# Kernel tuning notes

Measured on AMD Instinct MI355X. Metric: run time of the kernel, lower is better.

The kernel has to match this reference:

```python
import jax, jax.numpy as jnp
import numpy as np

EPS = 1e-5

def _bn(x, gamma, beta):
    # training-mode BatchNorm1d over (batch, points) per channel; x: [B, C, N]
    mean = x.mean(axis=(0, 2), keepdims=True)
    var = x.var(axis=(0, 2), keepdims=True)
    return gamma[None, :, None] * (x - mean) * jax.lax.rsqrt(var + EPS) + beta[None, :, None]

def _conv_nn(x, idx, W, b):
    # x: [B, Cin, N_in]; idx: [N_out, k]; W: [Cout, Cin, k]
    g = x[:, :, idx]  # gather -> [B, Cin, N_out, k]
    return jnp.einsum('bink,oik->bon', g, W) + b[None, :, None]

def setup_inputs() -> dict:
    key = jax.random.key(0)
    ks = jax.random.split(key, 8)
    B, Cin, Cout = 32, 32, 64
    Nin, Nout, K, KP = 32768, 8192, 9, 4
    s = 0.05
    return {
        'x': jax.random.normal(ks[0], (B, Cin, Nin), jnp.float32),
        'W1': jax.random.normal(ks[1], (Cout, Cin, K), jnp.float32) * s,
        'b1': jnp.zeros((Cout,), jnp.float32),
        'W2': jax.random.normal(ks[2], (Cout, Cout, K), jnp.float32) * s,
        'b2': jnp.zeros((Cout,), jnp.float32),
        'We': jax.random.normal(ks[3], (Cout, Cin), jnp.float32) * s,
        'be': jnp.zeros((Cout,), jnp.float32),
        'g1': jnp.ones((Cout,), jnp.float32), 'beta1': jnp.zeros((Cout,), jnp.float32),
        'g2': jnp.ones((Cout,), jnp.float32), 'beta2': jnp.zeros((Cout,), jnp.float32),
        'g3': jnp.ones((Cout,), jnp.float32), 'beta3': jnp.zeros((Cout,), jnp.float32),
        'idx1': jax.random.randint(ks[4], (Nout, K), 0, Nin, jnp.int32),
        'idx2': jax.random.randint(ks[5], (Nout, K), 0, Nout, jnp.int32),
        'pool_idx': jax.random.randint(ks[6], (Nout, KP), 0, Nin, jnp.int32),
    }

def reference(x, W1, b1, W2, b2, We, be, g1, beta1, g2, beta2, g3, beta3, idx1, idx2, pool_idx):
    # main branch: ConvNN -> BN -> ReLU -> ConvNN -> BN
    out = jax.nn.relu(_bn(_conv_nn(x, idx1, W1, b1), g1, beta1))
    out = _bn(_conv_nn(out, idx2, W2, b2), g2, beta2)
    # shortcut: AvgPoolNN (k=4) -> 1x1 conv expand -> BN
    pooled = x[:, :, pool_idx].mean(axis=-1)  # [B, Cin, N_out]
    identity = _bn(jnp.einsum('bin,oi->bon', pooled, We) + be[None, :, None], g3, beta3)
    return jax.nn.relu(out + identity)
```

## Files before the change

kernel.cpp:

```cpp
#include <hip/hip_runtime.h>

typedef __attribute__((ext_vector_type(8))) short short8_t;
typedef __attribute__((ext_vector_type(4))) float f32x4_t;

#define NOUT 8192
#define NIN 32768
#define MTOT 262144.0f
#define ST_STRIPES 64

static __device__ __forceinline__ float bf2f(ushort u) {
    union { float f; unsigned int i; } x; x.i = ((unsigned int)u) << 16; return x.f;
}
static __device__ __forceinline__ ushort f2bf(float f) {
    union { float f; unsigned int i; } x; x.f = f;
    unsigned int r = x.i + 0x7fffu + ((x.i >> 16) & 1u);
    return (ushort)(r >> 16);
}

__global__ __launch_bounds__(256) void transpose_x_kernel(
    const float* __restrict__ x, ushort* __restrict__ xt)
{
    __shared__ ushort T[64][66];
    const int tid = threadIdx.x;
    const int n0 = blockIdx.x * 64, c0 = blockIdx.y * 64;
    const int lane64 = tid & 63, rb = (tid >> 6) * 16;
    #pragma unroll
    for (int r = 0; r < 16; ++r) {
        int c_l = rb + r;
        T[c_l][lane64] = f2bf(x[(size_t)(c0 + c_l) * NIN + n0 + lane64]);
    }
    __syncthreads();
    #pragma unroll
    for (int r = 0; r < 16; ++r) {
        int n_l = rb + r;
        xt[(size_t)(n0 + n_l) * 1024 + c0 + lane64] = T[lane64][n_l];
    }
}

__global__ __launch_bounds__(256) void prep_w_kernel(
    const float* __restrict__ W1, const float* __restrict__ W2,
    const float* __restrict__ We,
    ushort* __restrict__ w1p, ushort* __restrict__ w2p, ushort* __restrict__ wep)
{
    int t = blockIdx.x * 256 + threadIdx.x;
    const int N1 = 9 * 64 * 32, N2 = 9 * 64 * 64, N3 = 64 * 32;
    if (t < N1) {
        int k = t >> 11, rem = t & 2047, o = rem >> 5, i = rem & 31;
        w1p[t] = f2bf(W1[o * 288 + i * 9 + k]);
    } else if (t < N1 + N2) {
        int t2 = t - N1;
        int k = t2 >> 12, rem = t2 & 4095, o = rem >> 6, ci = rem & 63;
        w2p[t2] = f2bf(W2[o * 576 + ci * 9 + k]);
    } else if (t < N1 + N2 + N3) {
        int t3 = t - N1 - N2;
        wep[t3] = f2bf(We[t3]);
    }
}

__global__ __launch_bounds__(256) void conv1_kernel(
    const ushort* __restrict__ xt, const int* __restrict__ idx1,
    const ushort* __restrict__ w1p, ushort* __restrict__ out1,
    float* __restrict__ st)
{
    __shared__ ushort As[128 * 40];
    __shared__ ushort Ws[64 * 40];
    __shared__ float Ls[128];
    const int tid = threadIdx.x;
    const int lane = tid & 63, wv = tid >> 6;
    const int nbase = blockIdx.x * 4;
    const int r_st = tid >> 1, h_st = tid & 1;
    const int nl_st = tid >> 6, b_st = r_st & 31;
    const int o_st = tid >> 2, sg_st = tid & 3;

    f32x4_t acc[2][4];
    #pragma unroll
    for (int m = 0; m < 2; ++m)
        #pragma unroll
        for (int nt = 0; nt < 4; ++nt) acc[m][nt] = (f32x4_t){0.f, 0.f, 0.f, 0.f};

    {
        int rrow = idx1[(nbase + nl_st) * 9];
        const int4* src = (const int4*)(xt + (size_t)rrow * 1024 + b_st * 32 + h_st * 16);
        int4* dst = (int4*)(As + r_st * 40 + h_st * 16);
        dst[0] = src[0]; dst[1] = src[1];
        const int4* wsrc = (const int4*)(w1p + o_st * 32 + sg_st * 8);
        *(int4*)(Ws + o_st * 40 + sg_st * 8) = wsrc[0];
    }
    if (tid < 128) Ls[tid] = 0.f;
    __syncthreads();

    for (int k = 0; k < 9; ++k) {
        int4 pa0, pa1, pw;
        const bool pre = (k + 1 < 9);
        if (pre) {
            int rrow = idx1[(nbase + nl_st) * 9 + k + 1];
            const int4* src = (const int4*)(xt + (size_t)rrow * 1024 + b_st * 32 + h_st * 16);
            pa0 = src[0]; pa1 = src[1];
            pw = *(const int4*)(w1p + (k + 1) * 2048 + o_st * 32 + sg_st * 8);
        }
        short8_t af[2], bfr[4];
        #pragma unroll
        for (int m = 0; m < 2; ++m)
            af[m] = *(const short8_t*)(As + (wv * 32 + m * 16 + (lane & 15)) * 40 + (lane >> 4) * 8);
        #pragma unroll
        for (int nt = 0; nt < 4; ++nt)
            bfr[nt] = *(const short8_t*)(Ws + (nt * 16 + (lane & 15)) * 40 + (lane >> 4) * 8);
        #pragma unroll
        for (int m = 0; m < 2; ++m)
            #pragma unroll
            for (int nt = 0; nt < 4; ++nt)
                acc[m][nt] = __builtin_amdgcn_mfma_f32_16x16x32_bf16(af[m], bfr[nt], acc[m][nt], 0, 0, 0);
        __syncthreads();
        if (pre) {
            int4* dst = (int4*)(As + r_st * 40 + h_st * 16);
            dst[0] = pa0; dst[1] = pa1;
            *(int4*)(Ws + o_st * 40 + sg_st * 8) = pw;
        }
        __syncthreads();
    }

    #pragma unroll
    for (int m = 0; m < 2; ++m)
        #pragma unroll
        for (int nt = 0; nt < 4; ++nt)
            #pragma unroll
            for (int j = 0; j < 4; ++j) {
                int row = wv * 32 + m * 16 + (lane >> 4) * 4 + j;
                int nl = row >> 5, bb = row & 31, col = nt * 16 + (lane & 15);
                out1[(size_t)(nbase + nl) * 2048 + bb * 64 + col] = f2bf(acc[m][nt][j]);
            }
    #pragma unroll
    for (int nt = 0; nt < 4; ++nt) {
        float s = 0.f, q = 0.f;
        #pragma unroll
        for (int m = 0; m < 2; ++m)
            #pragma unroll
            for (int j = 0; j < 4; ++j) { float v = acc[m][nt][j]; s += v; q += v * v; }
        s += __shfl_xor(s, 16); s += __shfl_xor(s, 32);
        q += __shfl_xor(q, 16); q += __shfl_xor(q, 32);
        if (lane < 16) {
            atomicAdd(&Ls[nt * 16 + lane], s);
            atomicAdd(&Ls[64 + nt * 16 + lane], q);
        }
    }
    __syncthreads();
    if (tid < 128) atomicAdd(&st[(blockIdx.x & (ST_STRIPES - 1)) * 128 + tid], Ls[tid]);
}

__global__ __launch_bounds__(256) void conv2_kernel(
    const ushort* __restrict__ out1n, const int* __restrict__ idx2,
    const ushort* __restrict__ w2p, ushort* __restrict__ out2,
    float* __restrict__ st)
{
    __shared__ ushort As[128 * 72];
    __shared__ ushort Ws[64 * 72];
    __shared__ float Ls[128];
    const int tid = threadIdx.x;
    const int lane = tid & 63, wv = tid >> 6;
    const int nbase = blockIdx.x * 4;
    const int r_st = tid >> 1, h_st = tid & 1;
    const int nl_st = tid >> 6, b_st = r_st & 31;
    const int o_st = tid >> 2, sg_st = tid & 3;

    f32x4_t acc[2][4];
    #pragma unroll
    for (int m = 0; m < 2; ++m)
        #pragma unroll
        for (int nt = 0; nt < 4; ++nt) acc[m][nt] = (f32x4_t){0.f, 0.f, 0.f, 0.f};

    {
        int rrow = idx2[(nbase + nl_st) * 9];
        const int4* src = (const int4*)(out1n + (size_t)rrow * 2048 + b_st * 64 + h_st * 32);
        int4* dst = (int4*)(As + r_st * 72 + h_st * 32);
        dst[0] = src[0]; dst[1] = src[1]; dst[2] = src[2]; dst[3] = src[3];
        const int4* wsrc = (const int4*)(w2p + o_st * 64 + sg_st * 16);
        int4* wdst = (int4*)(Ws + o_st * 72 + sg_st * 16);
        wdst[0] = wsrc[0]; wdst[1] = wsrc[1];
    }
    if (tid < 128) Ls[tid] = 0.f;
    __syncthreads();

    for (int k = 0; k < 9; ++k) {
        int4 pa0, pa1, pa2, pa3, pw0, pw1;
        const bool pre = (k + 1 < 9);
        if (pre) {
            int rrow = idx2[(nbase + nl_st) * 9 + k + 1];
            const int4* src = (const int4*)(out1n + (size_t)rrow * 2048 + b_st * 64 + h_st * 32);
            pa0 = src[0]; pa1 = src[1]; pa2 = src[2]; pa3 = src[3];
            const int4* wsrc = (const int4*)(w2p + (k + 1) * 4096 + o_st * 64 + sg_st * 16);
            pw0 = wsrc[0]; pw1 = wsrc[1];
        }
        #pragma unroll
        for (int kk = 0; kk < 2; ++kk) {
            short8_t af[2], bfr[4];
            #pragma unroll
            for (int m = 0; m < 2; ++m)
                af[m] = *(const short8_t*)(As + (wv * 32 + m * 16 + (lane & 15)) * 72 + kk * 32 + (lane >> 4) * 8);
            #pragma unroll
            for (int nt = 0; nt < 4; ++nt)
                bfr[nt] = *(const short8_t*)(Ws + (nt * 16 + (lane & 15)) * 72 + kk * 32 + (lane >> 4) * 8);
            #pragma unroll
            for (int m = 0; m < 2; ++m)
                #pragma unroll
                for (int nt = 0; nt < 4; ++nt)
                    acc[m][nt] = __builtin_amdgcn_mfma_f32_16x16x32_bf16(af[m], bfr[nt], acc[m][nt], 0, 0, 0);
        }
        __syncthreads();
        if (pre) {
            int4* dst = (int4*)(As + r_st * 72 + h_st * 32);
            dst[0] = pa0; dst[1] = pa1; dst[2] = pa2; dst[3] = pa3;
            int4* wdst = (int4*)(Ws + o_st * 72 + sg_st * 16);
            wdst[0] = pw0; wdst[1] = pw1;
        }
        __syncthreads();
    }

    #pragma unroll
    for (int m = 0; m < 2; ++m)
        #pragma unroll
        for (int nt = 0; nt < 4; ++nt)
            #pragma unroll
            for (int j = 0; j < 4; ++j) {
                int row = wv * 32 + m * 16 + (lane >> 4) * 4 + j;
                int nl = row >> 5, bb = row & 31, col = nt * 16 + (lane & 15);
                out2[(size_t)(nbase + nl) * 2048 + bb * 64 + col] = f2bf(acc[m][nt][j]);
            }
    #pragma unroll
    for (int nt = 0; nt < 4; ++nt) {
        float s = 0.f, q = 0.f;
        #pragma unroll
        for (int m = 0; m < 2; ++m)
            #pragma unroll
            for (int j = 0; j < 4; ++j) { float v = acc[m][nt][j]; s += v; q += v * v; }
        s += __shfl_xor(s, 16); s += __shfl_xor(s, 32);
        q += __shfl_xor(q, 16); q += __shfl_xor(q, 32);
        if (lane < 16) {
            atomicAdd(&Ls[nt * 16 + lane], s);
            atomicAdd(&Ls[64 + nt * 16 + lane], q);
        }
    }
    __syncthreads();
    if (tid < 128) atomicAdd(&st[(blockIdx.x & (ST_STRIPES - 1)) * 128 + tid], Ls[tid]);
}

__global__ __launch_bounds__(256) void ident_kernel(
    const ushort* __restrict__ xt, const int* __restrict__ pool_idx,
    const ushort* __restrict__ wep, ushort* __restrict__ identt,
    float* __restrict__ st)
{
    __shared__ ushort As[256 * 40];
    __shared__ ushort Ws[64 * 40];
    __shared__ float Ls[128];
    const int tid = threadIdx.x;
    const int lane = tid & 63, wv = tid >> 6;
    const int nbase = blockIdx.x * 8;
    const int n_l = tid >> 5, b = tid & 31;

    float pa[32];
    #pragma unroll
    for (int i = 0; i < 32; ++i) pa[i] = 0.f;
    for (int kp = 0; kp < 4; ++kp) {
        int rrow = pool_idx[(nbase + n_l) * 4 + kp];
        const int4* src = (const int4*)(xt + (size_t)rrow * 1024 + b * 32);
        #pragma unroll
        for (int j = 0; j < 4; ++j) {
            int4 v = src[j];
            const ushort* pv = (const ushort*)&v;
            #pragma unroll
            for (int e = 0; e < 8; ++e) pa[j * 8 + e] += bf2f(pv[e]);
        }
    }
    {
        int4* dst = (int4*)(As + (n_l * 32 + b) * 40);
        #pragma unroll
        for (int j = 0; j < 4; ++j) {
            int4 v; ushort* pv = (ushort*)&v;
            #pragma unroll
            for (int e = 0; e < 8; ++e) pv[e] = f2bf(pa[j * 8 + e] * 0.25f);
            dst[j] = v;
        }
    }
    {
        int o = tid >> 2, seg = tid & 3;
        *(int4*)(Ws + o * 40 + seg * 8) = *(const int4*)(wep + o * 32 + seg * 8);
    }
    if (tid < 128) Ls[tid] = 0.f;
    __syncthreads();

    f32x4_t acc[4][4];
    #pragma unroll
    for (int m = 0; m < 4; ++m)
        #pragma unroll
        for (int nt = 0; nt < 4; ++nt) acc[m][nt] = (f32x4_t){0.f, 0.f, 0.f, 0.f};
    short8_t af[4], bfr[4];
    #pragma unroll
    for (int m = 0; m < 4; ++m)
        af[m] = *(const short8_t*)(As + (wv * 64 + m * 16 + (lane & 15)) * 40 + (lane >> 4) * 8);
    #pragma unroll
    for (int nt = 0; nt < 4; ++nt)
        bfr[nt] = *(const short8_t*)(Ws + (nt * 16 + (lane & 15)) * 40 + (lane >> 4) * 8);
    #pragma unroll
    for (int m = 0; m < 4; ++m)
        #pragma unroll
        for (int nt = 0; nt < 4; ++nt)
            acc[m][nt] = __builtin_amdgcn_mfma_f32_16x16x32_bf16(af[m], bfr[nt], acc[m][nt], 0, 0, 0);

    #pragma unroll
    for (int m = 0; m < 4; ++m)
        #pragma unroll
        for (int nt = 0; nt < 4; ++nt)
            #pragma unroll
            for (int j = 0; j < 4; ++j) {
                int row = wv * 64 + m * 16 + (lane >> 4) * 4 + j;
                int nl = row >> 5, bb = row & 31, col = nt * 16 + (lane & 15);
                identt[(size_t)(nbase + nl) * 2048 + bb * 64 + col] = f2bf(acc[m][nt][j]);
            }
    #pragma unroll
    for (int nt = 0; nt < 4; ++nt) {
        float s = 0.f, q = 0.f;
        #pragma unroll
        for (int m = 0; m < 4; ++m)
            #pragma unroll
            for (int j = 0; j < 4; ++j) { float v = acc[m][nt][j]; s += v; q += v * v; }
        s += __shfl_xor(s, 16); s += __shfl_xor(s, 32);
        q += __shfl_xor(q, 16); q += __shfl_xor(q, 32);
        if (lane < 16) {
            atomicAdd(&Ls[nt * 16 + lane], s);
            atomicAdd(&Ls[64 + nt * 16 + lane], q);
        }
    }
    __syncthreads();
    if (tid < 128) atomicAdd(&st[(blockIdx.x & (ST_STRIPES - 1)) * 128 + tid], Ls[tid]);
}

__global__ void finalize_kernel(const float* __restrict__ st, const float* __restrict__ g,
                                const float* __restrict__ bet, float* __restrict__ ac)
{
    int o = threadIdx.x;
    if (o >= 64) return;
    float s = 0.f, q = 0.f;
    for (int i = 0; i < ST_STRIPES; ++i) { s += st[i * 128 + o]; q += st[i * 128 + 64 + o]; }
    float mean = s * (1.0f / MTOT);
    float var  = q * (1.0f / MTOT) - mean * mean;
    float a = g[o] * rsqrtf(var + 1e-5f);
    ac[o] = a;
    ac[64 + o] = bet[o] - a * mean;
}

__global__ __launch_bounds__(256) void bn_relu_ip_kernel(
    ushort* __restrict__ buf, const float* __restrict__ ac)
{
    const int tid = threadIdx.x;
    const int o0 = (tid * 8) & 63;
    float a[8], c[8];
    #pragma unroll
    for (int e = 0; e < 8; ++e) { a[e] = ac[o0 + e]; c[e] = ac[64 + o0 + e]; }
    size_t base = (size_t)(blockIdx.x * 256 + tid) * 8;
    const size_t stride = (size_t)1024 * 256 * 8;
    for (int it = 0; it < 8; ++it, base += stride) {
        int4 v = *(int4*)(buf + base);
        ushort* pv = (ushort*)&v;
        #pragma unroll
        for (int e = 0; e < 8; ++e) {
            float f = a[e] * bf2f(pv[e]) + c[e];
            pv[e] = f2bf(fmaxf(f, 0.f));
        }
        *(int4*)(buf + base) = v;
    }
}

__global__ __launch_bounds__(256) void final_combine_kernel(
    const ushort* __restrict__ out2, const ushort* __restrict__ idt,
    const float* __restrict__ ac2, const float* __restrict__ ac3,
    float* __restrict__ dout)
{
    __shared__ float tile[64][65];
    const int tid = threadIdx.x;
    const int n0 = blockIdx.x * 64, bo0 = blockIdx.y * 64;
    const int lane64 = tid & 63, rb = (tid >> 6) * 16;
    const int o = lane64;
    const float a2 = ac2[o], c2 = ac2[64 + o], a3 = ac3[o], c3 = ac3[64 + o];
    #pragma unroll
    for (int r = 0; r < 16; ++r) {
        int n_l = rb + r;
        size_t p = (size_t)(n0 + n_l) * 2048 + bo0 + lane64;
        float v = a2 * bf2f(out2[p]) + c2 + a3 * bf2f(idt[p]) + c3;
        tile[n_l][lane64] = fmaxf(v, 0.f);
    }
    __syncthreads();
    #pragma unroll
    for (int r = 0; r < 16; ++r) {
        int bo_l = rb + r;
        dout[(size_t)(bo0 + bo_l) * NOUT + n0 + lane64] = tile[lane64][bo_l];
    }
}

extern "C" void kernel_launch(void* const* d_in, const int* in_sizes, int n_in,
                              void* d_out, int out_size, void* d_ws, size_t ws_size,
                              hipStream_t stream)
{
    const float* x     = (const float*)d_in[0];
    const float* W1    = (const float*)d_in[1];
    const float* W2    = (const float*)d_in[3];
    const float* We    = (const float*)d_in[5];
    const float* g1    = (const float*)d_in[7];
    const float* beta1 = (const float*)d_in[8];
    const float* g2    = (const float*)d_in[9];
    const float* beta2 = (const float*)d_in[10];
    const float* g3    = (const float*)d_in[11];
    const float* beta3 = (const float*)d_in[12];
    const int* idx1    = (const int*)d_in[13];
    const int* idx2    = (const int*)d_in[14];
    const int* pool_idx= (const int*)d_in[15];
    float* dout = (float*)d_out;

    char* ws = (char*)d_ws;
    const size_t off_xt   = 0;
    const size_t off_out1 = 67108864;
    const size_t off_out2 = 100663296;
    const size_t off_id   = 134217728;
    const size_t off_w1p  = 167772160;
    const size_t off_w2p  = 167809024;
    const size_t off_wep  = 167882752;
    const size_t off_st   = 167886848;
    const size_t off_ac   = 167985152;
    const size_t need     = 167986688;
    if (ws_size < need) return;

    ushort* xt   = (ushort*)(ws + off_xt);
    ushort* out1 = (ushort*)(ws + off_out1);
    ushort* out2 = (ushort*)(ws + off_out2);
    ushort* idt  = (ushort*)(ws + off_id);
    ushort* w1p  = (ushort*)(ws + off_w1p);
    ushort* w2p  = (ushort*)(ws + off_w2p);
    ushort* wep  = (ushort*)(ws + off_wep);
    float*  st1  = (float*)(ws + off_st);
    float*  st2  = st1 + 64 * 128;
    float*  st3  = st1 + 2 * 64 * 128;
    float*  ac1  = (float*)(ws + off_ac);
    float*  ac2  = ac1 + 128;
    float*  ac3  = ac1 + 256;

    hipMemsetAsync(ws + off_st, 0, 3 * 64 * 128 * 4, stream);

    prep_w_kernel<<<224, 256, 0, stream>>>(W1, W2, We, w1p, w2p, wep);
    transpose_x_kernel<<<dim3(512, 16), 256, 0, stream>>>(x, xt);
    conv1_kernel<<<2048, 256, 0, stream>>>(xt, idx1, w1p, out1, st1);
    finalize_kernel<<<1, 64, 0, stream>>>(st1, g1, beta1, ac1);
    bn_relu_ip_kernel<<<1024, 256, 0, stream>>>(out1, ac1);
    conv2_kernel<<<2048, 256, 0, stream>>>(out1, idx2, w2p, out2, st2);
    ident_kernel<<<1024, 256, 0, stream>>>(xt, pool_idx, wep, idt, st3);
    finalize_kernel<<<1, 64, 0, stream>>>(st2, g2, beta2, ac2);
    finalize_kernel<<<1, 64, 0, stream>>>(st3, g3, beta3, ac3);
    final_combine_kernel<<<dim3(128, 32), 256, 0, stream>>>(out2, idt, ac2, ac3, dout);
}
```

Measured before the change: 192.2 us.

## Fuse BN1+ReLU into conv2 gather and merge small launches

Removes the standalone in-place BN+ReLU pass over out1 by applying the per-channel affine and ReLU to gathered rows inside conv2, after the MFMAs and before the LDS store. The stats memset is folded into prep_w_kernel and the two final finalize launches are merged into one two-block kernel. This drops a full read/write of the 32 MB out1 buffer and a few launches. The cost is that conv2 repeats the BN math for each of the 9 gathers of a row.

```diff
diff --git a/kernel.cpp b/kernel.cpp
--- a/kernel.cpp
+++ b/kernel.cpp
@@ -17,6 +17,16 @@
     return (ushort)(r >> 16);
 }
 
+static __device__ __forceinline__ int4 bnx(int4 v, const float* __restrict__ acs, int ch0) {
+    ushort* pv = (ushort*)&v;
+    #pragma unroll
+    for (int e = 0; e < 8; ++e) {
+        float f = acs[ch0 + e] * bf2f(pv[e]) + acs[64 + ch0 + e];
+        pv[e] = f2bf(fmaxf(f, 0.f));
+    }
+    return v;
+}
+
 __global__ __launch_bounds__(256) void transpose_x_kernel(
     const float* __restrict__ x, ushort* __restrict__ xt)
 {
@@ -40,10 +50,12 @@
 __global__ __launch_bounds__(256) void prep_w_kernel(
     const float* __restrict__ W1, const float* __restrict__ W2,
     const float* __restrict__ We,
-    ushort* __restrict__ w1p, ushort* __restrict__ w2p, ushort* __restrict__ wep)
+    ushort* __restrict__ w1p, ushort* __restrict__ w2p, ushort* __restrict__ wep,
+    float* __restrict__ stz)
 {
     int t = blockIdx.x * 256 + threadIdx.x;
     const int N1 = 9 * 64 * 32, N2 = 9 * 64 * 64, N3 = 64 * 32;
+    if (t < 3 * ST_STRIPES * 128) stz[t] = 0.f;
     if (t < N1) {
         int k = t >> 11, rem = t & 2047, o = rem >> 5, i = rem & 31;
         w1p[t] = f2bf(W1[o * 288 + i * 9 + k]);
@@ -148,19 +160,21 @@
 }
 
 __global__ __launch_bounds__(256) void conv2_kernel(
-    const ushort* __restrict__ out1n, const int* __restrict__ idx2,
-    const ushort* __restrict__ w2p, ushort* __restrict__ out2,
-    float* __restrict__ st)
+    const ushort* __restrict__ out1raw, const int* __restrict__ idx2,
+    const ushort* __restrict__ w2p, const float* __restrict__ ac1,
+    ushort* __restrict__ out2, float* __restrict__ st)
 {
     __shared__ ushort As[128 * 72];
     __shared__ ushort Ws[64 * 72];
     __shared__ float Ls[128];
+    __shared__ float ACs[128];
     const int tid = threadIdx.x;
     const int lane = tid & 63, wv = tid >> 6;
     const int nbase = blockIdx.x * 4;
     const int r_st = tid >> 1, h_st = tid & 1;
     const int nl_st = tid >> 6, b_st = r_st & 31;
     const int o_st = tid >> 2, sg_st = tid & 3;
+    const int ch0 = h_st * 32;
 
     f32x4_t acc[2][4];
     #pragma unroll
@@ -168,16 +182,25 @@
         #pragma unroll
         for (int nt = 0; nt < 4; ++nt) acc[m][nt] = (f32x4_t){0.f, 0.f, 0.f, 0.f};
 
+    if (tid < 128) { ACs[tid] = ac1[tid]; Ls[tid] = 0.f; }
+
+    int4 q0, q1, q2, q3;
     {
         int rrow = idx2[(nbase + nl_st) * 9];
-        const int4* src = (const int4*)(out1n + (size_t)rrow * 2048 + b_st * 64 + h_st * 32);
-        int4* dst = (int4*)(As + r_st * 72 + h_st * 32);
-        dst[0] = src[0]; dst[1] = src[1]; dst[2] = src[2]; dst[3] = src[3];
+        const int4* src = (const int4*)(out1raw + (size_t)rrow * 2048 + b_st * 64 + h_st * 32);
+        q0 = src[0]; q1 = src[1]; q2 = src[2]; q3 = src[3];
         const int4* wsrc = (const int4*)(w2p + o_st * 64 + sg_st * 16);
         int4* wdst = (int4*)(Ws + o_st * 72 + sg_st * 16);
         wdst[0] = wsrc[0]; wdst[1] = wsrc[1];
     }
-    if (tid < 128) Ls[tid] = 0.f;
+    __syncthreads();
+    {
+        int4* dst = (int4*)(As + r_st * 72 + h_st * 32);
+        dst[0] = bnx(q0, ACs, ch0);
+        dst[1] = bnx(q1, ACs, ch0 + 8);
+        dst[2] = bnx(q2, ACs, ch0 + 16);
+        dst[3] = bnx(q3, ACs, ch0 + 24);
+    }
     __syncthreads();
 
     for (int k = 0; k < 9; ++k) {
@@ -185,7 +208,7 @@
         const bool pre = (k + 1 < 9);
         if (pre) {
             int rrow = idx2[(nbase + nl_st) * 9 + k + 1];
-            const int4* src = (const int4*)(out1n + (size_t)rrow * 2048 + b_st * 64 + h_st * 32);
+            const int4* src = (const int4*)(out1raw + (size_t)rrow * 2048 + b_st * 64 + h_st * 32);
             pa0 = src[0]; pa1 = src[1]; pa2 = src[2]; pa3 = src[3];
             const int4* wsrc = (const int4*)(w2p + (k + 1) * 4096 + o_st * 64 + sg_st * 16);
             pw0 = wsrc[0]; pw1 = wsrc[1];
@@ -204,6 +227,12 @@
                 #pragma unroll
                 for (int nt = 0; nt < 4; ++nt)
                     acc[m][nt] = __builtin_amdgcn_mfma_f32_16x16x32_bf16(af[m], bfr[nt], acc[m][nt], 0, 0, 0);
+        }
+        if (pre) {
+            pa0 = bnx(pa0, ACs, ch0);
+            pa1 = bnx(pa1, ACs, ch0 + 8);
+            pa2 = bnx(pa2, ACs, ch0 + 16);
+            pa3 = bnx(pa3, ACs, ch0 + 24);
         }
         __syncthreads();
         if (pre) {
@@ -347,26 +376,24 @@
     ac[64 + o] = bet[o] - a * mean;
 }
 
-__global__ __launch_bounds__(256) void bn_relu_ip_kernel(
-    ushort* __restrict__ buf, const float* __restrict__ ac)
-{
-    const int tid = threadIdx.x;
-    const int o0 = (tid * 8) & 63;
-    float a[8], c[8];
-    #pragma unroll
-    for (int e = 0; e < 8; ++e) { a[e] = ac[o0 + e]; c[e] = ac[64 + o0 + e]; }
-    size_t base = (size_t)(blockIdx.x * 256 + tid) * 8;
-    const size_t stride = (size_t)1024 * 256 * 8;
-    for (int it = 0; it < 8; ++it, base += stride) {
-        int4 v = *(int4*)(buf + base);
-        ushort* pv = (ushort*)&v;
-        #pragma unroll
-        for (int e = 0; e < 8; ++e) {
-            float f = a[e] * bf2f(pv[e]) + c[e];
-            pv[e] = f2bf(fmaxf(f, 0.f));
-        }
-        *(int4*)(buf + base) = v;
-    }
+__global__ void finalize23_kernel(
+    const float* __restrict__ st2, const float* __restrict__ g2, const float* __restrict__ b2,
+    const float* __restrict__ st3, const float* __restrict__ g3, const float* __restrict__ b3,
+    float* __restrict__ ac2, float* __restrict__ ac3)
+{
+    int o = threadIdx.x;
+    if (o >= 64) return;
+    const float* st = blockIdx.x ? st3 : st2;
+    const float* g  = blockIdx.x ? g3  : g2;
+    const float* bt = blockIdx.x ? b3  : b2;
+    float* ac       = blockIdx.x ? ac3 : ac2;
+    float s = 0.f, q = 0.f;
+    for (int i = 0; i < ST_STRIPES; ++i) { s += st[i * 128 + o]; q += st[i * 128 + 64 + o]; }
+    float mean = s * (1.0f / MTOT);
+    float var  = q * (1.0f / MTOT) - mean * mean;
+    float a = g[o] * rsqrtf(var + 1e-5f);
+    ac[o] = a;
+    ac[64 + o] = bt[o] - a * mean;
 }
 
 __global__ __launch_bounds__(256) void final_combine_kernel(
@@ -441,16 +468,12 @@
     float*  ac2  = ac1 + 128;
     float*  ac3  = ac1 + 256;
 
-    hipMemsetAsync(ws + off_st, 0, 3 * 64 * 128 * 4, stream);
-
-    prep_w_kernel<<<224, 256, 0, stream>>>(W1, W2, We, w1p, w2p, wep);
+    prep_w_kernel<<<224, 256, 0, stream>>>(W1, W2, We, w1p, w2p, wep, st1);
     transpose_x_kernel<<<dim3(512, 16), 256, 0, stream>>>(x, xt);
     conv1_kernel<<<2048, 256, 0, stream>>>(xt, idx1, w1p, out1, st1);
+    ident_kernel<<<1024, 256, 0, stream>>>(xt, pool_idx, wep, idt, st3);
     finalize_kernel<<<1, 64, 0, stream>>>(st1, g1, beta1, ac1);
-    bn_relu_ip_kernel<<<1024, 256, 0, stream>>>(out1, ac1);
-    conv2_kernel<<<2048, 256, 0, stream>>>(out1, idx2, w2p, out2, st2);
-    ident_kernel<<<1024, 256, 0, stream>>>(xt, pool_idx, wep, idt, st3);
-    finalize_kernel<<<1, 64, 0, stream>>>(st2, g2, beta2, ac2);
-    finalize_kernel<<<1, 64, 0, stream>>>(st3, g3, beta3, ac3);
+    conv2_kernel<<<2048, 256, 0, stream>>>(out1, idx2, w2p, ac1, out2, st2);
+    finalize23_kernel<<<2, 64, 0, stream>>>(st2, g2, beta2, st3, g3, beta3, ac2, ac3);
     final_combine_kernel<<<dim3(128, 32), 256, 0, stream>>>(out2, idt, ac2, ac3, dout);
 }
```

New measurement: 191.0 us. No clear change (-0.7%).
